# Kernel tuning notes

Hardware: AMD Instinct MI355X
Metric: run time of the kernel (lower is better)

The kernel has to match this reference:

```python
import jax, jax.numpy as jnp
import numpy as np
from jax import lax

WS = 7  # window_size
PAD = WS // 2


def _gaussian_window(window_size, channel, sigma=1.5):
    x = np.arange(window_size, dtype=np.float64)
    g = np.exp(-((x - window_size // 2) ** 2) / (2.0 * sigma ** 2))
    g = g / g.sum()
    w2 = np.outer(g, g).astype(np.float32)  # (ws, ws)
    w = np.broadcast_to(w2[None, None], (channel, 1, window_size, window_size))
    return jnp.asarray(np.ascontiguousarray(w))


def setup_inputs() -> dict:
    key = jax.random.key(0)
    k1, k2, k3 = jax.random.split(key, 3)
    shape = (16, 1, 1024, 1024)
    img1 = jax.random.uniform(k1, shape, dtype=jnp.float32)
    img2 = jax.random.uniform(k2, shape, dtype=jnp.float32)
    img3 = jax.random.uniform(k3, shape, dtype=jnp.float32)
    window = _gaussian_window(WS, channel=1)  # (1,1,7,7) depthwise Gaussian
    return {"img1": img1, "img2": img2, "img3": img3, "window": window}


def _dwconv(x, window, channel):
    # depthwise conv2d, SAME-style padding = ws//2, groups = channel
    return lax.conv_general_dilated(
        x, window, window_strides=(1, 1), padding=[(PAD, PAD), (PAD, PAD)],
        dimension_numbers=("NCHW", "OIHW", "NCHW"), feature_group_count=channel)


def reference(img1, img2, img3, window):
    channel = img1.shape[1]
    conv = lambda x: _dwconv(x, window, channel)

    mu1 = conv(img1)
    mu2 = conv(img2)
    mu3 = conv(img3)

    sigma1_sq = conv(img1 * img1) - mu1 * mu1
    sigma2_sq = conv(img2 * img2) - mu2 * mu2
    sigma3_sq = conv(img3 * img3) - mu3 * mu3
    sigma12 = conv(img1 * img2) - mu1 * mu2
    sigma13 = conv(img1 * img3) - mu1 * mu3

    C2 = 0.03 ** 2
    ssim_map_12 = (2.0 * sigma12 + C2) / (sigma1_sq + sigma2_sq + C2)
    ssim_map_13 = (2.0 * sigma13 + C2) / (sigma1_sq + sigma3_sq + C2)

    # size_average=True branch
    ssim_map = jnp.where(mu2 > mu3, ssim_map_12, ssim_map_13)
    return jnp.mean(ssim_map)
```

## Files before the change

kernel.cpp:

```cpp
#include <hip/hip_runtime.h>

typedef float v2f __attribute__((ext_vector_type(2)));

#define W 1024
#define H 1024
#define NB 16
#define TX 32
#define TY 26
#define HR 32
#define NTH 256
#define YBLK ((H + TY - 1) / TY)
#define RSTRIDE (8 * TX)

template <int TALL>
__device__ __forceinline__ float vconv_ssim(
    const float* __restrict__ hbuf, int base, const float* __restrict__ g,
    int gy0 )
{
    v2f sv[4][TALL];
    #pragma unroll
    for (int cp = 0; cp < 4; ++cp)
        #pragma unroll
        for (int j = 0; j < TALL; ++j) sv[cp][j] = (v2f)0.0f;

    #pragma unroll
    for (int dy = 0; dy < TALL + 6; ++dy) {
        v2f p[4];
        #pragma unroll
        for (int cp = 0; cp < 4; ++cp) {
            p[cp].x = hbuf[base + cp * 64];
            p[cp].y = hbuf[base + cp * 64 + 32];
        }
        #pragma unroll
        for (int j = 0; j < TALL; ++j) {
            const int dd = dy - j;
            if (dd >= 0 && dd < 7) {
                const float wg = g[dd];
                #pragma unroll
                for (int cp = 0; cp < 4; ++cp) sv[cp][j] += wg * p[cp];
            }
        }
        base += RSTRIDE;
    }

    float lsum = 0.0f;
    #pragma unroll
    for (int j = 0; j < TALL; ++j) {
        if (gy0 + j < H) {
            const float mu1 = sv[0][j].x, mu2 = sv[0][j].y;
            const float mu3 = sv[1][j].x, E11 = sv[1][j].y;
            const float E22 = sv[2][j].x, E33 = sv[2][j].y;
            const float E12 = sv[3][j].x, E13 = sv[3][j].y;
            const float sig1  = E11 - mu1 * mu1;
            const float sig2  = E22 - mu2 * mu2;
            const float sig3  = E33 - mu3 * mu3;
            const float sig12 = E12 - mu1 * mu2;
            const float sig13 = E13 - mu1 * mu3;
            const float C2 = 9.0e-4f;
            const float m12 = (2.0f * sig12 + C2) * __builtin_amdgcn_rcpf(sig1 + sig2 + C2);
            const float m13 = (2.0f * sig13 + C2) * __builtin_amdgcn_rcpf(sig1 + sig3 + C2);
            lsum += (mu2 > mu3) ? m12 : m13;
        }
    }
    return lsum;
}

__global__ __launch_bounds__(NTH, 5) void ssim_main(
    const float* __restrict__ img1, const float* __restrict__ img2,
    const float* __restrict__ img3, const float* __restrict__ win,
    float* __restrict__ partial)
{
    __shared__ __align__(16) float hbuf[HR * RSTRIDE];

    const int tid = threadIdx.x;
    const int x0  = blockIdx.x * TX;
    const int ys0 = blockIdx.y * TY;
    const size_t imoff = (size_t)blockIdx.z * (size_t)(W * H);
    const float* p1 = img1 + imoff;
    const float* p2 = img2 + imoff;
    const float* p3 = img3 + imoff;

    float g[7];
    {
        const float inv = 1.0f / sqrtf(win[24]);
        #pragma unroll
        for (int j = 0; j < 7; ++j) g[j] = win[21 + j] * inv;
    }

    {
        const int br  = tid >> 3;
        const int bc0 = (tid & 7) << 2;
        const int gy  = ys0 + br - 3;
        const int gx0 = x0 + bc0 - 4;
        const bool xfast = (gx0 >= 0) & (gx0 + 12 <= W);

        v2f accA[8], accB[8];
        #pragma unroll
        for (int ch = 0; ch < 8; ++ch) { accA[ch] = (v2f)0.0f; accB[ch] = (v2f)0.0f; }

        if ((gy >= 0) & (gy < H)) {
            const size_t rowoff = (size_t)gy * W;
            float V1[12], V2[12], V3[12];
            if (xfast) {
                const float* q1 = p1 + rowoff + gx0;
                const float* q2 = p2 + rowoff + gx0;
                const float* q3 = p3 + rowoff + gx0;
                *(float4*)&V1[0] = *(const float4*)(q1);
                *(float4*)&V1[4] = *(const float4*)(q1 + 4);
                *(float4*)&V1[8] = *(const float4*)(q1 + 8);
                *(float4*)&V2[0] = *(const float4*)(q2);
                *(float4*)&V2[4] = *(const float4*)(q2 + 4);
                *(float4*)&V2[8] = *(const float4*)(q2 + 8);
                *(float4*)&V3[0] = *(const float4*)(q3);
                *(float4*)&V3[4] = *(const float4*)(q3 + 4);
                *(float4*)&V3[8] = *(const float4*)(q3 + 8);
            } else {
                #pragma unroll
                for (int c = 0; c < 12; ++c) {
                    const int x = gx0 + c;
                    const bool ok = (x >= 0) & (x < W);
                    const size_t off = rowoff + x;
                    V1[c] = ok ? p1[off] : 0.0f;
                    V2[c] = ok ? p2[off] : 0.0f;
                    V3[c] = ok ? p3[off] : 0.0f;
                }
            }

            v2f gp[8];
            gp[0] = (v2f){g[0], 0.0f};
            #pragma unroll
            for (int m = 2; m <= 7; ++m) gp[m - 1] = (v2f){g[m - 1], g[m - 2]};
            gp[7] = (v2f){0.0f, g[6]};

            #pragma unroll
            for (int m = 1; m <= 8; ++m) {
                const v2f w = gp[m - 1];
                const float vA1 = V1[m], vA2 = V2[m], vA3 = V3[m];
                const float vB1 = V1[m + 2], vB2 = V2[m + 2], vB3 = V3[m + 2];
                v2f t;
                t = w * vA1; accA[0] += t; accA[3] += t * vA1; accA[6] += t * vA2; accA[7] += t * vA3;
                t = w * vA2; accA[1] += t; accA[4] += t * vA2;
                t = w * vA3; accA[2] += t; accA[5] += t * vA3;
                t = w * vB1; accB[0] += t; accB[3] += t * vB1; accB[6] += t * vB2; accB[7] += t * vB3;
                t = w * vB2; accB[1] += t; accB[4] += t * vB2;
                t = w * vB3; accB[2] += t; accB[5] += t * vB3;
            }
        }
        const int wbase = br * RSTRIDE + bc0;
        #pragma unroll
        for (int ch = 0; ch < 8; ++ch) {
            *(v2f*)&hbuf[wbase + ch * TX]     = accA[ch];
            *(v2f*)&hbuf[wbase + ch * TX + 2] = accB[ch];
        }
    }
    __syncthreads();

    const int tx = tid & 31;
    float lsum;
    if (tid < 192) {
        const int r0 = (tid >> 5) * 3;
        lsum = vconv_ssim<3>(hbuf, r0 * RSTRIDE + tx, g, ys0 + r0);
    } else {
        const int r0 = 18 + (((tid >> 5) - 6) << 2);
        lsum = vconv_ssim<4>(hbuf, r0 * RSTRIDE + tx, g, ys0 + r0);
    }

    #pragma unroll
    for (int o = 32; o > 0; o >>= 1) lsum += __shfl_down(lsum, o, 64);
    __syncthreads();
    float* wavesum = hbuf;
    if ((tid & 63) == 0) wavesum[tid >> 6] = lsum;
    __syncthreads();
    if (tid == 0) {
        const float t = (wavesum[0] + wavesum[1]) + (wavesum[2] + wavesum[3]);
        partial[((size_t)blockIdx.z * gridDim.y + blockIdx.y) * gridDim.x + blockIdx.x] = t;
    }
}

__global__ __launch_bounds__(256) void ssim_reduce(
    const float* __restrict__ partial, float* __restrict__ out, int n)
{
    __shared__ double sh[256];
    const int tid = threadIdx.x;
    double s = 0.0;
    for (int i = tid; i < n; i += 256) s += (double)partial[i];
    sh[tid] = s;
    __syncthreads();
    for (int o = 128; o > 0; o >>= 1) {
        if (tid < o) sh[tid] += sh[tid + o];
        __syncthreads();
    }
    if (tid == 0) out[0] = (float)(sh[0] / (double)((size_t)NB * W * H));
}

extern "C" void kernel_launch(void* const* d_in, const int* in_sizes, int n_in,
                              void* d_out, int out_size, void* d_ws, size_t ws_size,
                              hipStream_t stream) {
    const float* img1 = (const float*)d_in[0];
    const float* img2 = (const float*)d_in[1];
    const float* img3 = (const float*)d_in[2];
    const float* win  = (const float*)d_in[3];
    float* out = (float*)d_out;
    float* partial = (float*)d_ws;

    dim3 grid(W / TX, YBLK, NB);
    ssim_main<<<grid, NTH, 0, stream>>>(img1, img2, img3, win, partial);

    const int nblk = (W / TX) * YBLK * NB;
    ssim_reduce<<<1, 256, 0, stream>>>(partial, out, nblk);
}
```

Baseline: 123.8 us.

## Interleave channel pairs in LDS and use packed FMA for vertical convolution

Shrinks the block tile height so every vertical-pass thread handles exactly three rows instead of a 3/4 row split. The horizontal pass now computes four outputs per thread with scalar FMAs and writes channel pairs interleaved into a padded LDS layout (row stride 260). This lets the vertical pass fetch each channel pair with one 64-bit LDS load and accumulate with inline-asm v_pk_fma_f32. The smaller tile adds more blocks and more halo overhead, and the horizontal pass loses its packed math.

```diff
diff --git a/kernel.cpp b/kernel.cpp
--- a/kernel.cpp
+++ b/kernel.cpp
@@ -6,63 +6,15 @@
 #define H 1024
 #define NB 16
 #define TX 32
-#define TY 26
-#define HR 32
+#define TY 24
+#define HR 30
 #define NTH 256
 #define YBLK ((H + TY - 1) / TY)
-#define RSTRIDE (8 * TX)
-
-template <int TALL>
-__device__ __forceinline__ float vconv_ssim(
-    const float* __restrict__ hbuf, int base, const float* __restrict__ g,
-    int gy0 )
-{
-    v2f sv[4][TALL];
-    #pragma unroll
-    for (int cp = 0; cp < 4; ++cp)
-        #pragma unroll
-        for (int j = 0; j < TALL; ++j) sv[cp][j] = (v2f)0.0f;
-
-    #pragma unroll
-    for (int dy = 0; dy < TALL + 6; ++dy) {
-        v2f p[4];
-        #pragma unroll
-        for (int cp = 0; cp < 4; ++cp) {
-            p[cp].x = hbuf[base + cp * 64];
-            p[cp].y = hbuf[base + cp * 64 + 32];
-        }
-        #pragma unroll
-        for (int j = 0; j < TALL; ++j) {
-            const int dd = dy - j;
-            if (dd >= 0 && dd < 7) {
-                const float wg = g[dd];
-                #pragma unroll
-                for (int cp = 0; cp < 4; ++cp) sv[cp][j] += wg * p[cp];
-            }
-        }
-        base += RSTRIDE;
-    }
-
-    float lsum = 0.0f;
-    #pragma unroll
-    for (int j = 0; j < TALL; ++j) {
-        if (gy0 + j < H) {
-            const float mu1 = sv[0][j].x, mu2 = sv[0][j].y;
-            const float mu3 = sv[1][j].x, E11 = sv[1][j].y;
-            const float E22 = sv[2][j].x, E33 = sv[2][j].y;
-            const float E12 = sv[3][j].x, E13 = sv[3][j].y;
-            const float sig1  = E11 - mu1 * mu1;
-            const float sig2  = E22 - mu2 * mu2;
-            const float sig3  = E33 - mu3 * mu3;
-            const float sig12 = E12 - mu1 * mu2;
-            const float sig13 = E13 - mu1 * mu3;
-            const float C2 = 9.0e-4f;
-            const float m12 = (2.0f * sig12 + C2) * __builtin_amdgcn_rcpf(sig1 + sig2 + C2);
-            const float m13 = (2.0f * sig13 + C2) * __builtin_amdgcn_rcpf(sig1 + sig3 + C2);
-            lsum += (mu2 > mu3) ? m12 : m13;
-        }
-    }
-    return lsum;
+#define CPSTRIDE 64
+#define RSTRIDE 260
+
+__device__ __forceinline__ v2f pk_fma(v2f a, v2f b, v2f c) {
+    v2f d; asm("v_pk_fma_f32 %0, %1, %2, %3" : "=v"(d) : "v"(a), "v"(b), "v"(c)); return d;
 }
 
 __global__ __launch_bounds__(NTH, 5) void ssim_main(
@@ -87,16 +39,18 @@
         for (int j = 0; j < 7; ++j) g[j] = win[21 + j] * inv;
     }
 
-    {
+    if (tid < HR * 8) {
         const int br  = tid >> 3;
         const int bc0 = (tid & 7) << 2;
         const int gy  = ys0 + br - 3;
         const int gx0 = x0 + bc0 - 4;
         const bool xfast = (gx0 >= 0) & (gx0 + 12 <= W);
 
-        v2f accA[8], accB[8];
-        #pragma unroll
-        for (int ch = 0; ch < 8; ++ch) { accA[ch] = (v2f)0.0f; accB[ch] = (v2f)0.0f; }
+        float acc[8][4];
+        #pragma unroll
+        for (int ch = 0; ch < 8; ++ch)
+            #pragma unroll
+            for (int j = 0; j < 4; ++j) acc[ch][j] = 0.0f;
 
         if ((gy >= 0) & (gy < H)) {
             const size_t rowoff = (size_t)gy * W;
@@ -125,44 +79,91 @@
                     V3[c] = ok ? p3[off] : 0.0f;
                 }
             }
-
-            v2f gp[8];
-            gp[0] = (v2f){g[0], 0.0f};
-            #pragma unroll
-            for (int m = 2; m <= 7; ++m) gp[m - 1] = (v2f){g[m - 1], g[m - 2]};
-            gp[7] = (v2f){0.0f, g[6]};
-
-            #pragma unroll
-            for (int m = 1; m <= 8; ++m) {
-                const v2f w = gp[m - 1];
-                const float vA1 = V1[m], vA2 = V2[m], vA3 = V3[m];
-                const float vB1 = V1[m + 2], vB2 = V2[m + 2], vB3 = V3[m + 2];
-                v2f t;
-                t = w * vA1; accA[0] += t; accA[3] += t * vA1; accA[6] += t * vA2; accA[7] += t * vA3;
-                t = w * vA2; accA[1] += t; accA[4] += t * vA2;
-                t = w * vA3; accA[2] += t; accA[5] += t * vA3;
-                t = w * vB1; accB[0] += t; accB[3] += t * vB1; accB[6] += t * vB2; accB[7] += t * vB3;
-                t = w * vB2; accB[1] += t; accB[4] += t * vB2;
-                t = w * vB3; accB[2] += t; accB[5] += t * vB3;
-            }
-        }
-        const int wbase = br * RSTRIDE + bc0;
-        #pragma unroll
-        for (int ch = 0; ch < 8; ++ch) {
-            *(v2f*)&hbuf[wbase + ch * TX]     = accA[ch];
-            *(v2f*)&hbuf[wbase + ch * TX + 2] = accB[ch];
-        }
-    }
-    __syncthreads();
-
-    const int tx = tid & 31;
-    float lsum;
-    if (tid < 192) {
-        const int r0 = (tid >> 5) * 3;
-        lsum = vconv_ssim<3>(hbuf, r0 * RSTRIDE + tx, g, ys0 + r0);
-    } else {
-        const int r0 = 18 + (((tid >> 5) - 6) << 2);
-        lsum = vconv_ssim<4>(hbuf, r0 * RSTRIDE + tx, g, ys0 + r0);
+            #pragma unroll
+            for (int j = 0; j < 4; ++j) {
+                #pragma unroll
+                for (int dx = 0; dx < 7; ++dx) {
+                    const float w  = g[dx];
+                    const float v1 = V1[1 + j + dx];
+                    const float v2 = V2[1 + j + dx];
+                    const float v3 = V3[1 + j + dx];
+                    const float t1 = w * v1;
+                    const float t2 = w * v2;
+                    const float t3 = w * v3;
+                    acc[0][j] += t1;
+                    acc[1][j] += t2;
+                    acc[2][j] += t3;
+                    acc[3][j] += t1 * v1;
+                    acc[4][j] += t2 * v2;
+                    acc[5][j] += t3 * v3;
+                    acc[6][j] += t1 * v2;
+                    acc[7][j] += t1 * v3;
+                }
+            }
+        }
+        const int wbase = br * RSTRIDE + bc0 * 2;
+        #pragma unroll
+        for (int cp = 0; cp < 4; ++cp) {
+            float* d = &hbuf[wbase + cp * CPSTRIDE];
+            *(float4*)(d + 0) = make_float4(acc[2 * cp][0], acc[2 * cp + 1][0],
+                                            acc[2 * cp][1], acc[2 * cp + 1][1]);
+            *(float4*)(d + 4) = make_float4(acc[2 * cp][2], acc[2 * cp + 1][2],
+                                            acc[2 * cp][3], acc[2 * cp + 1][3]);
+        }
+    }
+    __syncthreads();
+
+    const int tx  = tid & 31;
+    const int r0  = (tid >> 5) * 3;
+    float lsum = 0.0f;
+    {
+        v2f gb[7];
+        #pragma unroll
+        for (int d = 0; d < 7; ++d) { gb[d].x = g[d]; gb[d].y = g[d]; }
+
+        v2f sv[4][3];
+        #pragma unroll
+        for (int cp = 0; cp < 4; ++cp)
+            #pragma unroll
+            for (int j = 0; j < 3; ++j) sv[cp][j] = (v2f)0.0f;
+
+        int base = r0 * RSTRIDE + tx * 2;
+        #pragma unroll
+        for (int dy = 0; dy < 9; ++dy) {
+            v2f p[4];
+            #pragma unroll
+            for (int cp = 0; cp < 4; ++cp)
+                p[cp] = *(const v2f*)&hbuf[base + cp * CPSTRIDE];
+            #pragma unroll
+            for (int j = 0; j < 3; ++j) {
+                const int dd = dy - j;
+                if (dd >= 0 && dd < 7) {
+                    #pragma unroll
+                    for (int cp = 0; cp < 4; ++cp)
+                        sv[cp][j] = pk_fma(p[cp], gb[dd], sv[cp][j]);
+                }
+            }
+            base += RSTRIDE;
+        }
+
+        #pragma unroll
+        for (int j = 0; j < 3; ++j) {
+            if (ys0 + r0 + j < H) {
+                const float mu1 = sv[0][j].x, mu2 = sv[0][j].y;
+                const float mu3 = sv[1][j].x, E11 = sv[1][j].y;
+                const float E22 = sv[2][j].x, E33 = sv[2][j].y;
+                const float E12 = sv[3][j].x, E13 = sv[3][j].y;
+                const float sig1  = E11 - mu1 * mu1;
+                const float sig2  = E22 - mu2 * mu2;
+                const float sig3  = E33 - mu3 * mu3;
+                const float sig12 = E12 - mu1 * mu2;
+                const float sig13 = E13 - mu1 * mu3;
+                const float C2 = 9.0e-4f;
+                const float m12 = (2.0f * sig12 + C2) * __builtin_amdgcn_rcpf(sig1 + sig2 + C2);
+                const float m13 = (2.0f * sig13 + C2) * __builtin_amdgcn_rcpf(sig1 + sig3 + C2);
+                lsum += (mu2 > mu3) ? m12 : m13;
+            }
+        }
     }
 
     #pragma unroll
```

After: 242.0 us. +95.6%, slower.
